# Kernel optimization log

Hardware: AMD Instinct MI355X
Metric: run time of the kernel (lower is better)

Reference implementation:

```python
import jax, jax.numpy as jnp
import numpy as np

VOCAB, B, T, H, E = 32000, 32, 128, 128, 128

def setup_inputs() -> dict:
    key = jax.random.key(0)
    ks = jax.random.split(key, 10)
    s = 0.05
    return {
        "inputs": jax.random.randint(ks[0], (B, T), 0, VOCAB, dtype=jnp.int32),
        "emb": jax.random.normal(ks[1], (VOCAB, E), jnp.float32) * s,
        "W0": jax.random.normal(ks[2], (E, 4 * H), jnp.float32) * s,
        "U0": jax.random.normal(ks[3], (H, 4 * H), jnp.float32) * s,
        "b0": jnp.zeros((4 * H,), jnp.float32),
        "W1": jax.random.normal(ks[4], (H, 4 * H), jnp.float32) * s,
        "U1": jax.random.normal(ks[5], (H, 4 * H), jnp.float32) * s,
        "b1": jnp.zeros((4 * H,), jnp.float32),
        "Wd": jax.random.normal(ks[6], (H, VOCAB), jnp.float32) * s,
        "bd": jnp.zeros((VOCAB,), jnp.float32),
    }

def _lstm_cell(x, h, c, W, U, b):
    # Keras LSTMCell gate order: i, f, c(candidate), o
    z = x @ W + h @ U + b  # [B, 4H]
    zi, zf, zc, zo = jnp.split(z, 4, axis=-1)
    i = jax.nn.sigmoid(zi)
    f = jax.nn.sigmoid(zf)
    o = jax.nn.sigmoid(zo)
    c_new = f * c + i * jnp.tanh(zc)
    h_new = o * jnp.tanh(c_new)
    return h_new, c_new

def reference(inputs, emb, W0, U0, b0, W1, U1, b1, Wd, bd):
    x = emb[inputs]  # [B, T, E]
    xt = jnp.transpose(x, (1, 0, 2))  # [T, B, E]
    zeros = jnp.zeros((x.shape[0], H), x.dtype)
    init = (zeros, zeros, zeros, zeros)  # h0, c0, h1, c1

    def step(carry, x_t):
        h0, c0, h1, c1 = carry
        h0, c0 = _lstm_cell(x_t, h0, c0, W0, U0, b0)
        h1, c1 = _lstm_cell(h0, h1, c1, W1, U1, b1)
        return (h0, c0, h1, c1), h1

    _, ys = jax.lax.scan(step, init, xt)  # ys: [T, B, H]
    y = jnp.transpose(ys, (1, 0, 2))  # [B, T, H]
    logits = y @ Wd + bd  # [B, T, VOCAB]
    return logits
```

## Files before the change

kernel.cpp:

```cpp
#include <hip/hip_runtime.h>
#include <math.h>

#define BB 32
#define TT 128
#define EE 128
#define HD 128
#define G4 512
#define NV 32000

typedef _Float16 f16x2  __attribute__((ext_vector_type(2)));
typedef _Float16 f16x4v __attribute__((ext_vector_type(4)));
typedef _Float16 f16x8  __attribute__((ext_vector_type(8)));
typedef float    f32x4  __attribute__((ext_vector_type(4)));

__global__ __launch_bounds__(256) void k_prep(
    const int* __restrict__ inputs, const float* __restrict__ emb,
    const float* __restrict__ W0, const float* __restrict__ b0,
    float* __restrict__ Z0x,
    const float* __restrict__ Wd, _Float16* __restrict__ Whi, _Float16* __restrict__ Wlo)
{
    if (blockIdx.x < 2000) {
        if (Whi == nullptr) return;
        const int g = blockIdx.x * 256 + threadIdx.x;
        const int chunk = g >> 6;
        const int lane = g & 63;
        const int ntile = chunk >> 2;
        const int kstep = chunk & 3;
        const int n = ntile * 16 + (lane & 15);
        const int kb = kstep * 32 + (lane >> 4) * 8;
        _Float16 hi[8], lo[8];
        #pragma unroll
        for (int j = 0; j < 8; ++j) {
            float v = Wd[(size_t)(kb + j) * NV + n];
            hi[j] = (_Float16)v;
            lo[j] = (_Float16)(v - (float)hi[j]);
        }
        *(float4*)&Whi[(size_t)chunk * 512 + lane * 8] = *(const float4*)hi;
        *(float4*)&Wlo[(size_t)chunk * 512 + lane * 8] = *(const float4*)lo;
        return;
    }
    __shared__ float xs[8][EE];
    const int r0 = (blockIdx.x - 2000) * 8;
    const int tid = threadIdx.x;
    for (int i = tid; i < 8 * EE; i += 256) {
        int r = i >> 7, e = i & 127;
        int tok = inputs[r0 + r];
        xs[r][e] = emb[tok * EE + e];
    }
    __syncthreads();
    const int c2 = tid * 2;
    float2 bb2 = *(const float2*)&b0[c2];
    float acc[8][2];
    #pragma unroll
    for (int r = 0; r < 8; ++r) { acc[r][0] = bb2.x; acc[r][1] = bb2.y; }
    for (int e = 0; e < EE; ++e) {
        float2 w = *(const float2*)&W0[e * G4 + c2];
        #pragma unroll
        for (int r = 0; r < 8; ++r) {
            float x = xs[r][e];
            acc[r][0] = fmaf(x, w.x, acc[r][0]);
            acc[r][1] = fmaf(x, w.y, acc[r][1]);
        }
    }
    #pragma unroll
    for (int r = 0; r < 8; ++r) {
        float2 o2; o2.x = acc[r][0]; o2.y = acc[r][1];
        *(float2*)&Z0x[(size_t)(r0 + r) * G4 + c2] = o2;
    }
}

__device__ __forceinline__ float sigf(float x) {
    return __builtin_amdgcn_rcpf(1.f + __builtin_amdgcn_exp2f(x * -1.44269504088896f));
}
__device__ __forceinline__ float tanh_f(float x) {
    return 1.f - 2.f * __builtin_amdgcn_rcpf(1.f + __builtin_amdgcn_exp2f(x * 2.88539008177793f));
}
__device__ __forceinline__ f16x8 ldfrag(const float* __restrict__ M, int col, int k0) {
    f16x8 v;
    #pragma unroll
    for (int j = 0; j < 8; ++j) v[j] = (_Float16)M[(size_t)(k0 + j) * G4 + col];
    return v;
}

#define REP8(X) X(0) X(1) X(2) X(3) X(4) X(5) X(6) X(7)

#define MFMA(acc, a, b) acc = __builtin_amdgcn_mfma_f32_16x16x32_f16(a, b, acc, 0, 0, 0)

#define DECLF(n) f16x8 u0_##n##_0, u0_##n##_1, u0_##n##_2, u0_##n##_3, \
                       w1_##n##_0, w1_##n##_1, w1_##n##_2, w1_##n##_3, \
                       u1_##n##_0, u1_##n##_1, u1_##n##_2, u1_##n##_3;

#define LOADF(n) { const int cn = wc0 + (n) * 16 + lo16; \
    u0_##n##_0 = ldfrag(U0, cn, khi);      u0_##n##_1 = ldfrag(U0, cn, 32 + khi); \
    u0_##n##_2 = ldfrag(U0, cn, 64 + khi); u0_##n##_3 = ldfrag(U0, cn, 96 + khi); \
    w1_##n##_0 = ldfrag(W1, cn, khi);      w1_##n##_1 = ldfrag(W1, cn, 32 + khi); \
    w1_##n##_2 = ldfrag(W1, cn, 64 + khi); w1_##n##_3 = ldfrag(W1, cn, 96 + khi); \
    asm("" : "+a"(w1_##n##_0), "+a"(w1_##n##_1), "+a"(w1_##n##_2), "+a"(w1_##n##_3)); \
    u1_##n##_0 = ldfrag(U1, cn, khi);      u1_##n##_1 = ldfrag(U1, cn, 32 + khi); \
    u1_##n##_2 = ldfrag(U1, cn, 64 + khi); u1_##n##_3 = ldfrag(U1, cn, 96 + khi); \
    asm("" : "+a"(u1_##n##_0), "+a"(u1_##n##_1), "+a"(u1_##n##_2), "+a"(u1_##n##_3)); }

#define PA(n) { f32x4 acc = {0.f, 0.f, 0.f, 0.f}; \
    MFMA(acc, ha0, u0_##n##_0); MFMA(acc, ha1, u0_##n##_1); \
    MFMA(acc, ha2, u0_##n##_2); MFMA(acc, ha3, u0_##n##_3); \
    if (lane < 32) { const int cw = wc0 + (n) * 16 + lo16; const int br = (lane >> 4) * 4; \
        zbuf[br + 0][cw] = acc[0]; zbuf[br + 1][cw] = acc[1]; \
        zbuf[br + 2][cw] = acc[2]; zbuf[br + 3][cw] = acc[3]; } }

#define PC(n) { f32x4 acc = {0.f, 0.f, 0.f, 0.f}; \
    MFMA(acc, ha0, w1_##n##_0); MFMA(acc, ha1, w1_##n##_1); \
    MFMA(acc, ha2, w1_##n##_2); MFMA(acc, ha3, w1_##n##_3); \
    MFMA(acc, hb0, u1_##n##_0); MFMA(acc, hb1, u1_##n##_1); \
    MFMA(acc, hb2, u1_##n##_2); MFMA(acc, hb3, u1_##n##_3); \
    if (lane < 32) { const int cw = wc0 + (n) * 16 + lo16; const int br = (lane >> 4) * 4; \
        zbuf[br + 0][cw] = acc[0]; zbuf[br + 1][cw] = acc[1]; \
        zbuf[br + 2][cw] = acc[2]; zbuf[br + 3][cw] = acc[3]; } }

#define GT0(K, ZI, ZF, ZC, ZO) { \
    float ig = sigf(ZI), fg = sigf(ZF), og = sigf(ZO), gg = tanh_f(ZC); \
    float cn = fg * c0v[K] + ig * gg; c0v[K] = cn; hv[K] = (_Float16)(og * tanh_f(cn)); }

#define GT1(K, ZI, ZF, ZC, ZO, YO) { \
    float ig = sigf(ZI), fg = sigf(ZF), og = sigf(ZO), gg = tanh_f(ZC); \
    float cn = fg * c1v[K] + ig * gg; c1v[K] = cn; float hn = og * tanh_f(cn); \
    hv[K] = (_Float16)hn; YO = hn; }

__global__ __launch_bounds__(256, 1) void k_lstm_m(
    const float* __restrict__ Z0x,
    const float* __restrict__ U0, const float* __restrict__ W1,
    const float* __restrict__ U1, const float* __restrict__ b1,
    float* __restrict__ y)
{
    const int tid  = threadIdx.x;
    const int lane = tid & 63;
    const int wc0  = (tid >> 6) * 128;
    const int lo16 = lane & 15;
    const int khi  = (lane >> 4) * 8;
    const int B0   = blockIdx.x * 8;

    __shared__ float     zbuf[8][516];
    __shared__ _Float16  h0p[16][136];
    __shared__ _Float16  h1p[16][136];

    REP8(DECLF)
    REP8(LOADF)

    const int bq  = tid >> 5;
    const int h0i = (tid & 31) * 4;
    const float* zx_base = Z0x + ((size_t)(B0 + bq) * TT) * G4;
    float*       y_base  = y   + ((size_t)(B0 + bq) * TT) * HD + h0i;

    const float4 b1_i = *(const float4*)&b1[0 * 128 + h0i];
    const float4 b1_f = *(const float4*)&b1[1 * 128 + h0i];
    const float4 b1_c = *(const float4*)&b1[2 * 128 + h0i];
    const float4 b1_o = *(const float4*)&b1[3 * 128 + h0i];

    for (int i = tid; i < 16 * 136; i += 256) {
        ((_Float16*)h0p)[i] = (_Float16)0.f;
        ((_Float16*)h1p)[i] = (_Float16)0.f;
    }
    f32x4 c0v = {0.f, 0.f, 0.f, 0.f};
    f32x4 c1v = {0.f, 0.f, 0.f, 0.f};
    __syncthreads();

    for (int t = 0; t < TT; ++t) {
        const float* zx = zx_base + (size_t)t * G4;
        const float4 x_i = *(const float4*)&zx[0 * 128 + h0i];
        const float4 x_f = *(const float4*)&zx[1 * 128 + h0i];
        const float4 x_c = *(const float4*)&zx[2 * 128 + h0i];
        const float4 x_o = *(const float4*)&zx[3 * 128 + h0i];

        {
            f16x8 ha0 = *(const f16x8*)&h0p[lo16][khi];
            f16x8 ha1 = *(const f16x8*)&h0p[lo16][32 + khi];
            f16x8 ha2 = *(const f16x8*)&h0p[lo16][64 + khi];
            f16x8 ha3 = *(const f16x8*)&h0p[lo16][96 + khi];
            REP8(PA)
        }
        __syncthreads();

        {
            const float4 zi4 = *(const float4*)&zbuf[bq][0 * 128 + h0i];
            const float4 zf4 = *(const float4*)&zbuf[bq][1 * 128 + h0i];
            const float4 zc4 = *(const float4*)&zbuf[bq][2 * 128 + h0i];
            const float4 zo4 = *(const float4*)&zbuf[bq][3 * 128 + h0i];
            f16x4v hv;
            GT0(0, zi4.x + x_i.x, zf4.x + x_f.x, zc4.x + x_c.x, zo4.x + x_o.x)
            GT0(1, zi4.y + x_i.y, zf4.y + x_f.y, zc4.y + x_c.y, zo4.y + x_o.y)
            GT0(2, zi4.z + x_i.z, zf4.z + x_f.z, zc4.z + x_c.z, zo4.z + x_o.z)
            GT0(3, zi4.w + x_i.w, zf4.w + x_f.w, zc4.w + x_c.w, zo4.w + x_o.w)
            *(f16x4v*)&h0p[bq][h0i] = hv;
        }
        __syncthreads();

        {
            f16x8 ha0 = *(const f16x8*)&h0p[lo16][khi];
            f16x8 ha1 = *(const f16x8*)&h0p[lo16][32 + khi];
            f16x8 ha2 = *(const f16x8*)&h0p[lo16][64 + khi];
            f16x8 ha3 = *(const f16x8*)&h0p[lo16][96 + khi];
            f16x8 hb0 = *(const f16x8*)&h1p[lo16][khi];
            f16x8 hb1 = *(const f16x8*)&h1p[lo16][32 + khi];
            f16x8 hb2 = *(const f16x8*)&h1p[lo16][64 + khi];
            f16x8 hb3 = *(const f16x8*)&h1p[lo16][96 + khi];
            REP8(PC)
        }
        __syncthreads();

        {
            const float4 zi4 = *(const float4*)&zbuf[bq][0 * 128 + h0i];
            const float4 zf4 = *(const float4*)&zbuf[bq][1 * 128 + h0i];
            const float4 zc4 = *(const float4*)&zbuf[bq][2 * 128 + h0i];
            const float4 zo4 = *(const float4*)&zbuf[bq][3 * 128 + h0i];
            f16x4v hv; float4 yv;
            GT1(0, zi4.x + b1_i.x, zf4.x + b1_f.x, zc4.x + b1_c.x, zo4.x + b1_o.x, yv.x)
            GT1(1, zi4.y + b1_i.y, zf4.y + b1_f.y, zc4.y + b1_c.y, zo4.y + b1_o.y, yv.y)
            GT1(2, zi4.z + b1_i.z, zf4.z + b1_f.z, zc4.z + b1_c.z, zo4.z + b1_o.z, yv.z)
            GT1(3, zi4.w + b1_i.w, zf4.w + b1_f.w, zc4.w + b1_c.w, zo4.w + b1_o.w, yv.w)
            *(f16x4v*)&h1p[bq][h0i] = hv;
            *(float4*)(y_base + (size_t)t * HD) = yv;
        }
        __syncthreads();
    }
}

__global__ __launch_bounds__(256) void k_ysplit(
    const float* __restrict__ y, _Float16* __restrict__ yhi, _Float16* __restrict__ ylo)
{
    const int g = blockIdx.x * 256 + threadIdx.x;
    const int chunk = g >> 6;
    const int lane = g & 63;
    const int mtile = chunk >> 2;
    const int kstep = chunk & 3;
    const int row = mtile * 16 + (lane & 15);
    const int kb = kstep * 32 + (lane >> 4) * 8;
    _Float16 hi[8], lo[8];
    #pragma unroll
    for (int j = 0; j < 8; ++j) {
        float v = y[(size_t)row * HD + kb + j];
        hi[j] = (_Float16)v;
        lo[j] = (_Float16)(v - (float)hi[j]);
    }
    *(float4*)&yhi[(size_t)chunk * 512 + lane * 8] = *(const float4*)hi;
    *(float4*)&ylo[(size_t)chunk * 512 + lane * 8] = *(const float4*)lo;
}

__global__ __launch_bounds__(256) void k_dense_mfma(
    const _Float16* __restrict__ yhi, const _Float16* __restrict__ ylo,
    const _Float16* __restrict__ Whi, const _Float16* __restrict__ Wlo,
    const float* __restrict__ bd, float* __restrict__ out)
{
    const int tid = threadIdx.x;
    const int w = tid >> 6;
    const int lane = tid & 63;
    const int mtile = blockIdx.x * 4 + w;
    const int nt0 = blockIdx.y * 20;

    f16x8 Ah[4], Al[4];
    #pragma unroll
    for (int k = 0; k < 4; ++k) {
        Ah[k] = *(const f16x8*)&yhi[(size_t)(mtile * 4 + k) * 512 + lane * 8];
        Al[k] = *(const f16x8*)&ylo[(size_t)(mtile * 4 + k) * 512 + lane * 8];
    }

    const int m0 = mtile * 16;
    const int r0 = (lane >> 4) * 4;

    for (int nt = 0; nt < 20; ++nt) {
        const int ntile = nt0 + nt;
        const size_t cbb = (size_t)ntile * 4 * 512 + lane * 8;
        f16x8 Bh[4], Bl[4];
        #pragma unroll
        for (int k = 0; k < 4; ++k) {
            Bh[k] = *(const f16x8*)&Whi[cbb + k * 512];
            Bl[k] = *(const f16x8*)&Wlo[cbb + k * 512];
        }
        f32x4 acc0 = {0.f, 0.f, 0.f, 0.f};
        f32x4 acc1 = {0.f, 0.f, 0.f, 0.f};
        #pragma unroll
        for (int k = 0; k < 4; ++k) {
            acc0 = __builtin_amdgcn_mfma_f32_16x16x32_f16(Ah[k], Bh[k], acc0, 0, 0, 0);
            acc1 = __builtin_amdgcn_mfma_f32_16x16x32_f16(Ah[k], Bl[k], acc1, 0, 0, 0);
            acc1 = __builtin_amdgcn_mfma_f32_16x16x32_f16(Al[k], Bh[k], acc1, 0, 0, 0);
        }
        const int col = ntile * 16 + (lane & 15);
        const float bias = bd[col];
        #pragma unroll
        for (int reg = 0; reg < 4; ++reg) {
            out[(size_t)(m0 + r0 + reg) * NV + col] = acc0[reg] + acc1[reg] + bias;
        }
    }
}

__global__ __launch_bounds__(256) void k_dense(
    const float* __restrict__ y, const float* __restrict__ Wd,
    const float* __restrict__ bd, float* __restrict__ out)
{
    __shared__ float ys[64 * HD];
    const int r0 = blockIdx.x * 64;
    const int v0 = blockIdx.y * 128;
    const int tid = threadIdx.x;
    for (int idx = tid; idx < 64 * HD; idx += 256) ys[idx] = y[(size_t)r0 * HD + idx];
    __syncthreads();
    const int tx = tid & 31;
    const int ty = tid >> 5;
    const int v = v0 + tx * 4;
    float4 bd4 = *(const float4*)&bd[v];
    float acc[8][4] = {};
    const float* yrow = &ys[(ty * 8) * HD];
    #pragma unroll 4
    for (int e = 0; e < HD; ++e) {
        float4 wv = *(const float4*)&Wd[(size_t)e * NV + v];
        #pragma unroll
        for (int j = 0; j < 8; ++j) {
            float yv = yrow[j * HD + e];
            acc[j][0] = fmaf(yv, wv.x, acc[j][0]);
            acc[j][1] = fmaf(yv, wv.y, acc[j][1]);
            acc[j][2] = fmaf(yv, wv.z, acc[j][2]);
            acc[j][3] = fmaf(yv, wv.w, acc[j][3]);
        }
    }
    #pragma unroll
    for (int j = 0; j < 8; ++j) {
        int rr = r0 + ty * 8 + j;
        float4 o4;
        o4.x = acc[j][0] + bd4.x;
        o4.y = acc[j][1] + bd4.y;
        o4.z = acc[j][2] + bd4.z;
        o4.w = acc[j][3] + bd4.w;
        *(float4*)&out[(size_t)rr * NV + v] = o4;
    }
}

extern "C" void kernel_launch(void* const* d_in, const int* in_sizes, int n_in,
                              void* d_out, int out_size, void* d_ws, size_t ws_size,
                              hipStream_t stream)
{
    const int*   inputs = (const int*)  d_in[0];
    const float* emb    = (const float*)d_in[1];
    const float* W0     = (const float*)d_in[2];
    const float* U0     = (const float*)d_in[3];
    const float* b0     = (const float*)d_in[4];
    const float* W1     = (const float*)d_in[5];
    const float* U1     = (const float*)d_in[6];
    const float* b1     = (const float*)d_in[7];
    const float* Wd     = (const float*)d_in[8];
    const float* bd     = (const float*)d_in[9];
    float* out = (float*)d_out;

    const size_t Z0X_B = (size_t)8 * 1024 * 1024;
    const size_t YY_B  = (size_t)2 * 1024 * 1024;
    const size_t WSP_B = (size_t)8000 * 512 * 2;
    const size_t YSP_B = (size_t)1024 * 512 * 2;
    const size_t NEED  = Z0X_B + YY_B + 2 * WSP_B + 2 * YSP_B + 4096;

    char* ws = (char*)d_ws;

    if (ws_size >= NEED) {
        float*     Z0x = (float*)ws;
        float*     yy  = (float*)(ws + Z0X_B);
        _Float16*  Whi = (_Float16*)(ws + Z0X_B + YY_B);
        _Float16*  Wlo = (_Float16*)(ws + Z0X_B + YY_B + WSP_B);
        _Float16*  yhi = (_Float16*)(ws + Z0X_B + YY_B + 2 * WSP_B);
        _Float16*  ylo = (_Float16*)(ws + Z0X_B + YY_B + 2 * WSP_B + YSP_B);

        k_prep<<<2512, 256, 0, stream>>>(inputs, emb, W0, b0, Z0x, Wd, Whi, Wlo);
        k_lstm_m<<<4, 256, 0, stream>>>(Z0x, U0, W1, U1, b1, yy);
        k_ysplit<<<256, 256, 0, stream>>>(yy, yhi, ylo);
        k_dense_mfma<<<dim3(64, 100), 256, 0, stream>>>(yhi, ylo, Whi, Wlo, bd, out);
    } else {
        float* yy = (float*)ws;
        size_t out_bytes = (size_t)out_size * sizeof(float);
        float* Z0x = (float*)((char*)d_out + out_bytes - Z0X_B);

        k_prep<<<2512, 256, 0, stream>>>(inputs, emb, W0, b0, Z0x,
                                         Wd, nullptr, nullptr);
        k_lstm_m<<<4, 256, 0, stream>>>(Z0x, U0, W1, U1, b1, yy);
        k_dense<<<dim3(64, 250), 256, 0, stream>>>(yy, Wd, bd, out);
    }
}
```

Baseline: 606.8 us.

## Compute LSTM gates in registers with column-aligned ownership and double-buffered h

```diff
diff --git a/kernel.cpp b/kernel.cpp
--- a/kernel.cpp
+++ b/kernel.cpp
@@ -83,14 +83,16 @@
 }
 
 #define REP8(X) X(0) X(1) X(2) X(3) X(4) X(5) X(6) X(7)
-
 #define MFMA(acc, a, b) acc = __builtin_amdgcn_mfma_f32_16x16x32_f16(a, b, acc, 0, 0, 0)
+#define TSTR (TT * G4)
 
 #define DECLF(n) f16x8 u0_##n##_0, u0_##n##_1, u0_##n##_2, u0_##n##_3, \
                        w1_##n##_0, w1_##n##_1, w1_##n##_2, w1_##n##_3, \
-                       u1_##n##_0, u1_##n##_1, u1_##n##_2, u1_##n##_3;
-
-#define LOADF(n) { const int cn = wc0 + (n) * 16 + lo16; \
+                       u1_##n##_0, u1_##n##_1, u1_##n##_2, u1_##n##_3; \
+                 f32x4 aU1_##n, aZ_##n; float b1c_##n; int col_##n;
+
+#define LOADF(n) { col_##n = ((n) >> 1) * 128 + wu + ((n) & 1) * 16 + lo16; \
+    const int cn = col_##n; \
     u0_##n##_0 = ldfrag(U0, cn, khi);      u0_##n##_1 = ldfrag(U0, cn, 32 + khi); \
     u0_##n##_2 = ldfrag(U0, cn, 64 + khi); u0_##n##_3 = ldfrag(U0, cn, 96 + khi); \
     w1_##n##_0 = ldfrag(W1, cn, khi);      w1_##n##_1 = ldfrag(W1, cn, 32 + khi); \
@@ -98,34 +100,37 @@
     asm("" : "+a"(w1_##n##_0), "+a"(w1_##n##_1), "+a"(w1_##n##_2), "+a"(w1_##n##_3)); \
     u1_##n##_0 = ldfrag(U1, cn, khi);      u1_##n##_1 = ldfrag(U1, cn, 32 + khi); \
     u1_##n##_2 = ldfrag(U1, cn, 64 + khi); u1_##n##_3 = ldfrag(U1, cn, 96 + khi); \
-    asm("" : "+a"(u1_##n##_0), "+a"(u1_##n##_1), "+a"(u1_##n##_2), "+a"(u1_##n##_3)); }
-
-#define PA(n) { f32x4 acc = {0.f, 0.f, 0.f, 0.f}; \
-    MFMA(acc, ha0, u0_##n##_0); MFMA(acc, ha1, u0_##n##_1); \
-    MFMA(acc, ha2, u0_##n##_2); MFMA(acc, ha3, u0_##n##_3); \
-    if (lane < 32) { const int cw = wc0 + (n) * 16 + lo16; const int br = (lane >> 4) * 4; \
-        zbuf[br + 0][cw] = acc[0]; zbuf[br + 1][cw] = acc[1]; \
-        zbuf[br + 2][cw] = acc[2]; zbuf[br + 3][cw] = acc[3]; } }
-
-#define PC(n) { f32x4 acc = {0.f, 0.f, 0.f, 0.f}; \
-    MFMA(acc, ha0, w1_##n##_0); MFMA(acc, ha1, w1_##n##_1); \
-    MFMA(acc, ha2, w1_##n##_2); MFMA(acc, ha3, w1_##n##_3); \
-    MFMA(acc, hb0, u1_##n##_0); MFMA(acc, hb1, u1_##n##_1); \
-    MFMA(acc, hb2, u1_##n##_2); MFMA(acc, hb3, u1_##n##_3); \
-    if (lane < 32) { const int cw = wc0 + (n) * 16 + lo16; const int br = (lane >> 4) * 4; \
-        zbuf[br + 0][cw] = acc[0]; zbuf[br + 1][cw] = acc[1]; \
-        zbuf[br + 2][cw] = acc[2]; zbuf[br + 3][cw] = acc[3]; } }
-
-#define GT0(K, ZI, ZF, ZC, ZO) { \
-    float ig = sigf(ZI), fg = sigf(ZF), og = sigf(ZO), gg = tanh_f(ZC); \
-    float cn = fg * c0v[K] + ig * gg; c0v[K] = cn; hv[K] = (_Float16)(og * tanh_f(cn)); }
-
-#define GT1(K, ZI, ZF, ZC, ZO, YO) { \
-    float ig = sigf(ZI), fg = sigf(ZF), og = sigf(ZO), gg = tanh_f(ZC); \
-    float cn = fg * c1v[K] + ig * gg; c1v[K] = cn; float hn = og * tanh_f(cn); \
-    hv[K] = (_Float16)hn; YO = hn; }
-
-__global__ __launch_bounds__(256, 1) void k_lstm_m(
+    asm("" : "+a"(u1_##n##_0), "+a"(u1_##n##_1), "+a"(u1_##n##_2), "+a"(u1_##n##_3)); \
+    b1c_##n = b1[cn]; }
+
+#define PU1(n) { f32x4 a = {0.f, 0.f, 0.f, 0.f}; \
+    MFMA(a, hb0, u1_##n##_0); MFMA(a, hb1, u1_##n##_1); \
+    MFMA(a, hb2, u1_##n##_2); MFMA(a, hb3, u1_##n##_3); aU1_##n = a; }
+
+#define PU0(n) { const float* zc = zxt + col_##n; f32x4 a; \
+    a[0] = zc[0]; a[1] = zc[TSTR]; a[2] = zc[2 * TSTR]; a[3] = zc[3 * TSTR]; \
+    MFMA(a, ha0, u0_##n##_0); MFMA(a, ha1, u0_##n##_1); \
+    MFMA(a, ha2, u0_##n##_2); MFMA(a, ha3, u0_##n##_3); aZ_##n = a; }
+
+#define PW1(n) { f32x4 a = {b1c_##n, b1c_##n, b1c_##n, b1c_##n}; \
+    MFMA(a, ha0, w1_##n##_0); MFMA(a, ha1, w1_##n##_1); \
+    MFMA(a, ha2, w1_##n##_2); MFMA(a, ha3, w1_##n##_3); \
+    aZ_##n = a + aU1_##n; }
+
+#define G0R(nI, nF, nC, nO, CS, h, r) { \
+    float ig = sigf(aZ_##nI[r]), fg = sigf(aZ_##nF[r]), og = sigf(aZ_##nO[r]); \
+    float gg = tanh_f(aZ_##nC[r]); \
+    float cn = fg * CS[r] + ig * gg; CS[r] = cn; \
+    h0c[bq4 + r][wu + lo16 + 16 * (h)] = (_Float16)(og * tanh_f(cn)); }
+
+#define G1R(nI, nF, nC, nO, CS, h, r) { \
+    float ig = sigf(aZ_##nI[r]), fg = sigf(aZ_##nF[r]), og = sigf(aZ_##nO[r]); \
+    float gg = tanh_f(aZ_##nC[r]); \
+    float cn = fg * CS[r] + ig * gg; CS[r] = cn; float hn = og * tanh_f(cn); \
+    h1c[bq4 + r][wu + lo16 + 16 * (h)] = (_Float16)hn; \
+    yb[(size_t)(r) * TT * HD + (size_t)t * HD + 16 * (h)] = hn; }
+
+__global__ __launch_bounds__(256, 1) void k_lstm_m2(
     const float* __restrict__ Z0x,
     const float* __restrict__ U0, const float* __restrict__ W1,
     const float* __restrict__ U1, const float* __restrict__ b1,
@@ -133,91 +138,71 @@
 {
     const int tid  = threadIdx.x;
     const int lane = tid & 63;
-    const int wc0  = (tid >> 6) * 128;
+    const int wu   = (tid >> 6) * 32;
     const int lo16 = lane & 15;
     const int khi  = (lane >> 4) * 8;
     const int B0   = blockIdx.x * 8;
-
-    __shared__ float     zbuf[8][516];
-    __shared__ _Float16  h0p[16][136];
-    __shared__ _Float16  h1p[16][136];
+    const int bq4  = (lane >> 4) * 4;
+    const int xr   = ((lane >> 4) & 1) * 4;
+
+    __shared__ _Float16 h0p[2][16][136];
+    __shared__ _Float16 h1p[2][16][136];
 
     REP8(DECLF)
     REP8(LOADF)
 
-    const int bq  = tid >> 5;
-    const int h0i = (tid & 31) * 4;
-    const float* zx_base = Z0x + ((size_t)(B0 + bq) * TT) * G4;
-    float*       y_base  = y   + ((size_t)(B0 + bq) * TT) * HD + h0i;
-
-    const float4 b1_i = *(const float4*)&b1[0 * 128 + h0i];
-    const float4 b1_f = *(const float4*)&b1[1 * 128 + h0i];
-    const float4 b1_c = *(const float4*)&b1[2 * 128 + h0i];
-    const float4 b1_o = *(const float4*)&b1[3 * 128 + h0i];
-
-    for (int i = tid; i < 16 * 136; i += 256) {
-        ((_Float16*)h0p)[i] = (_Float16)0.f;
-        ((_Float16*)h1p)[i] = (_Float16)0.f;
-    }
-    f32x4 c0v = {0.f, 0.f, 0.f, 0.f};
-    f32x4 c1v = {0.f, 0.f, 0.f, 0.f};
+    const float* zx0 = Z0x + ((size_t)(B0 + xr) * TT) * G4;
+    float* yb = y + ((size_t)(B0 + bq4) * TT) * HD + wu + lo16;
+
+    f32x4 c0a = {0.f,0.f,0.f,0.f}, c0b = {0.f,0.f,0.f,0.f};
+    f32x4 c1a = {0.f,0.f,0.f,0.f}, c1b = {0.f,0.f,0.f,0.f};
+
+    for (int i = tid; i < 2 * 16 * 136; i += 256) {
+        (&h0p[0][0][0])[i] = (_Float16)0.f;
+        (&h1p[0][0][0])[i] = (_Float16)0.f;
+    }
     __syncthreads();
 
     for (int t = 0; t < TT; ++t) {
-        const float* zx = zx_base + (size_t)t * G4;
-        const float4 x_i = *(const float4*)&zx[0 * 128 + h0i];
-        const float4 x_f = *(const float4*)&zx[1 * 128 + h0i];
-        const float4 x_c = *(const float4*)&zx[2 * 128 + h0i];
-        const float4 x_o = *(const float4*)&zx[3 * 128 + h0i];
+        const int p = t & 1;
+        const _Float16 (*h0r)[136] = h0p[p ^ 1];
+        const _Float16 (*h1r)[136] = h1p[p ^ 1];
+        _Float16 (*h0c)[136] = h0p[p];
+        _Float16 (*h1c)[136] = h1p[p];
+        const float* zxt = zx0 + (size_t)t * G4;
 
         {
-            f16x8 ha0 = *(const f16x8*)&h0p[lo16][khi];
-            f16x8 ha1 = *(const f16x8*)&h0p[lo16][32 + khi];
-            f16x8 ha2 = *(const f16x8*)&h0p[lo16][64 + khi];
-            f16x8 ha3 = *(const f16x8*)&h0p[lo16][96 + khi];
-            REP8(PA)
+            f16x8 hb0 = *(const f16x8*)&h1r[lo16][khi];
+            f16x8 hb1 = *(const f16x8*)&h1r[lo16][32 + khi];
+            f16x8 hb2 = *(const f16x8*)&h1r[lo16][64 + khi];
+            f16x8 hb3 = *(const f16x8*)&h1r[lo16][96 + khi];
+            REP8(PU1)
+            f16x8 ha0 = *(const f16x8*)&h0r[lo16][khi];
+            f16x8 ha1 = *(const f16x8*)&h0r[lo16][32 + khi];
+            f16x8 ha2 = *(const f16x8*)&h0r[lo16][64 + khi];
+            f16x8 ha3 = *(const f16x8*)&h0r[lo16][96 + khi];
+            REP8(PU0)
+        }
+        if (lane < 32) {
+            G0R(0, 2, 4, 6, c0a, 0, 0) G0R(0, 2, 4, 6, c0a, 0, 1)
+            G0R(0, 2, 4, 6, c0a, 0, 2) G0R(0, 2, 4, 6, c0a, 0, 3)
+            G0R(1, 3, 5, 7, c0b, 1, 0) G0R(1, 3, 5, 7, c0b, 1, 1)
+            G0R(1, 3, 5, 7, c0b, 1, 2) G0R(1, 3, 5, 7, c0b, 1, 3)
         }
         __syncthreads();
 
         {
-            const float4 zi4 = *(const float4*)&zbuf[bq][0 * 128 + h0i];
-            const float4 zf4 = *(const float4*)&zbuf[bq][1 * 128 + h0i];
-            const float4 zc4 = *(const float4*)&zbuf[bq][2 * 128 + h0i];
-            const float4 zo4 = *(const float4*)&zbuf[bq][3 * 128 + h0i];
-            f16x4v hv;
-            GT0(0, zi4.x + x_i.x, zf4.x + x_f.x, zc4.x + x_c.x, zo4.x + x_o.x)
-            GT0(1, zi4.y + x_i.y, zf4.y + x_f.y, zc4.y + x_c.y, zo4.y + x_o.y)
-            GT0(2, zi4.z + x_i.z, zf4.z + x_f.z, zc4.z + x_c.z, zo4.z + x_o.z)
-            GT0(3, zi4.w + x_i.w, zf4.w + x_f.w, zc4.w + x_c.w, zo4.w + x_o.w)
-            *(f16x4v*)&h0p[bq][h0i] = hv;
-        }
-        __syncthreads();
-
-        {
-            f16x8 ha0 = *(const f16x8*)&h0p[lo16][khi];
-            f16x8 ha1 = *(const f16x8*)&h0p[lo16][32 + khi];
-            f16x8 ha2 = *(const f16x8*)&h0p[lo16][64 + khi];
-            f16x8 ha3 = *(const f16x8*)&h0p[lo16][96 + khi];
-            f16x8 hb0 = *(const f16x8*)&h1p[lo16][khi];
-            f16x8 hb1 = *(const f16x8*)&h1p[lo16][32 + khi];
-            f16x8 hb2 = *(const f16x8*)&h1p[lo16][64 + khi];
-            f16x8 hb3 = *(const f16x8*)&h1p[lo16][96 + khi];
-            REP8(PC)
-        }
-        __syncthreads();
-
-        {
-            const float4 zi4 = *(const float4*)&zbuf[bq][0 * 128 + h0i];
-            const float4 zf4 = *(const float4*)&zbuf[bq][1 * 128 + h0i];
-            const float4 zc4 = *(const float4*)&zbuf[bq][2 * 128 + h0i];
-            const float4 zo4 = *(const float4*)&zbuf[bq][3 * 128 + h0i];
-            f16x4v hv; float4 yv;
-            GT1(0, zi4.x + b1_i.x, zf4.x + b1_f.x, zc4.x + b1_c.x, zo4.x + b1_o.x, yv.x)
-            GT1(1, zi4.y + b1_i.y, zf4.y + b1_f.y, zc4.y + b1_c.y, zo4.y + b1_o.y, yv.y)
-            GT1(2, zi4.z + b1_i.z, zf4.z + b1_f.z, zc4.z + b1_c.z, zo4.z + b1_o.z, yv.z)
-            GT1(3, zi4.w + b1_i.w, zf4.w + b1_f.w, zc4.w + b1_c.w, zo4.w + b1_o.w, yv.w)
-            *(f16x4v*)&h1p[bq][h0i] = hv;
-            *(float4*)(y_base + (size_t)t * HD) = yv;
+            f16x8 ha0 = *(const f16x8*)&h0c[lo16][khi];
+            f16x8 ha1 = *(const f16x8*)&h0c[lo16][32 + khi];
+            f16x8 ha2 = *(const f16x8*)&h0c[lo16][64 + khi];
+            f16x8 ha3 = *(const f16x8*)&h0c[lo16][96 + khi];
+            REP8(PW1)
+        }
+        if (lane < 32) {
+            G1R(0, 2, 4, 6, c1a, 0, 0) G1R(0, 2, 4, 6, c1a, 0, 1)
+            G1R(0, 2, 4, 6, c1a, 0, 2) G1R(0, 2, 4, 6, c1a, 0, 3)
+            G1R(1, 3, 5, 7, c1b, 1, 0) G1R(1, 3, 5, 7, c1b, 1, 1)
+            G1R(1, 3, 5, 7, c1b, 1, 2) G1R(1, 3, 5, 7, c1b, 1, 3)
         }
         __syncthreads();
     }
@@ -364,7 +349,7 @@
         _Float16*  ylo = (_Float16*)(ws + Z0X_B + YY_B + 2 * WSP_B + YSP_B);
 
         k_prep<<<2512, 256, 0, stream>>>(inputs, emb, W0, b0, Z0x, Wd, Whi, Wlo);
-        k_lstm_m<<<4, 256, 0, stream>>>(Z0x, U0, W1, U1, b1, yy);
+        k_lstm_m2<<<4, 256, 0, stream>>>(Z0x, U0, W1, U1, b1, yy);
         k_ysplit<<<256, 256, 0, stream>>>(yy, yhi, ylo);
         k_dense_mfma<<<dim3(64, 100), 256, 0, stream>>>(yhi, ylo, Whi, Wlo, bd, out);
     } else {
@@ -374,7 +359,7 @@
 
         k_prep<<<2512, 256, 0, stream>>>(inputs, emb, W0, b0, Z0x,
                                          Wd, nullptr, nullptr);
-        k_lstm_m<<<4, 256, 0, stream>>>(Z0x, U0, W1, U1, b1, yy);
+        k_lstm_m2<<<4, 256, 0, stream>>>(Z0x, U0, W1, U1, b1, yy);
         k_dense<<<dim3(64, 250), 256, 0, stream>>>(yy, Wd, bd, out);
     }
 }
```

Measured after the change: 946.2 us. 1.56x slower.

## Overlap Wd split with LSTM recurrence and retile dense MFMA to reuse B

Applied to the files above, without the earlier changes.

```diff
diff --git a/kernel.cpp b/kernel.cpp
--- a/kernel.cpp
+++ b/kernel.cpp
@@ -13,34 +13,13 @@
 typedef _Float16 f16x8  __attribute__((ext_vector_type(8)));
 typedef float    f32x4  __attribute__((ext_vector_type(4)));
 
-__global__ __launch_bounds__(256) void k_prep(
+__global__ __launch_bounds__(256) void k_embed(
     const int* __restrict__ inputs, const float* __restrict__ emb,
     const float* __restrict__ W0, const float* __restrict__ b0,
-    float* __restrict__ Z0x,
-    const float* __restrict__ Wd, _Float16* __restrict__ Whi, _Float16* __restrict__ Wlo)
-{
-    if (blockIdx.x < 2000) {
-        if (Whi == nullptr) return;
-        const int g = blockIdx.x * 256 + threadIdx.x;
-        const int chunk = g >> 6;
-        const int lane = g & 63;
-        const int ntile = chunk >> 2;
-        const int kstep = chunk & 3;
-        const int n = ntile * 16 + (lane & 15);
-        const int kb = kstep * 32 + (lane >> 4) * 8;
-        _Float16 hi[8], lo[8];
-        #pragma unroll
-        for (int j = 0; j < 8; ++j) {
-            float v = Wd[(size_t)(kb + j) * NV + n];
-            hi[j] = (_Float16)v;
-            lo[j] = (_Float16)(v - (float)hi[j]);
-        }
-        *(float4*)&Whi[(size_t)chunk * 512 + lane * 8] = *(const float4*)hi;
-        *(float4*)&Wlo[(size_t)chunk * 512 + lane * 8] = *(const float4*)lo;
-        return;
-    }
+    float* __restrict__ Z0x)
+{
     __shared__ float xs[8][EE];
-    const int r0 = (blockIdx.x - 2000) * 8;
+    const int r0 = blockIdx.x * 8;
     const int tid = threadIdx.x;
     for (int i = tid; i < 8 * EE; i += 256) {
         int r = i >> 7, e = i & 127;
@@ -83,7 +62,6 @@
 }
 
 #define REP8(X) X(0) X(1) X(2) X(3) X(4) X(5) X(6) X(7)
-
 #define MFMA(acc, a, b) acc = __builtin_amdgcn_mfma_f32_16x16x32_f16(a, b, acc, 0, 0, 0)
 
 #define DECLF(n) f16x8 u0_##n##_0, u0_##n##_1, u0_##n##_2, u0_##n##_3, \
@@ -125,13 +103,36 @@
     float cn = fg * c1v[K] + ig * gg; c1v[K] = cn; float hn = og * tanh_f(cn); \
     hv[K] = (_Float16)hn; YO = hn; }
 
-__global__ __launch_bounds__(256, 1) void k_lstm_m(
+__global__ __launch_bounds__(256, 1) void k_lstm_mw(
     const float* __restrict__ Z0x,
     const float* __restrict__ U0, const float* __restrict__ W1,
     const float* __restrict__ U1, const float* __restrict__ b1,
-    float* __restrict__ y)
+    float* __restrict__ y,
+    const float* __restrict__ Wd, _Float16* __restrict__ Whi, _Float16* __restrict__ Wlo)
 {
     const int tid  = threadIdx.x;
+
+    if (blockIdx.x >= 4) {
+        if (Whi == nullptr) return;
+        const int g = (blockIdx.x - 4) * 256 + tid;
+        const int chunk = g >> 6;
+        const int ln = g & 63;
+        const int ntile = chunk >> 2;
+        const int kstep = chunk & 3;
+        const int n = ntile * 16 + (ln & 15);
+        const int kb = kstep * 32 + (ln >> 4) * 8;
+        _Float16 hi[8], lo[8];
+        #pragma unroll
+        for (int j = 0; j < 8; ++j) {
+            float v = Wd[(size_t)(kb + j) * NV + n];
+            hi[j] = (_Float16)v;
+            lo[j] = (_Float16)(v - (float)hi[j]);
+        }
+        *(float4*)&Whi[(size_t)chunk * 512 + ln * 8] = *(const float4*)hi;
+        *(float4*)&Wlo[(size_t)chunk * 512 + ln * 8] = *(const float4*)lo;
+        return;
+    }
+
     const int lane = tid & 63;
     const int wc0  = (tid >> 6) * 128;
     const int lo16 = lane & 15;
@@ -244,49 +245,78 @@
     *(float4*)&ylo[(size_t)chunk * 512 + lane * 8] = *(const float4*)lo;
 }
 
-__global__ __launch_bounds__(256) void k_dense_mfma(
+__global__ __launch_bounds__(256) void k_dense_mfma2(
     const _Float16* __restrict__ yhi, const _Float16* __restrict__ ylo,
     const _Float16* __restrict__ Whi, const _Float16* __restrict__ Wlo,
     const float* __restrict__ bd, float* __restrict__ out)
 {
-    const int tid = threadIdx.x;
-    const int w = tid >> 6;
+    const int tid  = threadIdx.x;
+    const int w    = tid >> 6;
     const int lane = tid & 63;
-    const int mtile = blockIdx.x * 4 + w;
-    const int nt0 = blockIdx.y * 20;
-
-    f16x8 Ah[4], Al[4];
-    #pragma unroll
-    for (int k = 0; k < 4; ++k) {
-        Ah[k] = *(const f16x8*)&yhi[(size_t)(mtile * 4 + k) * 512 + lane * 8];
-        Al[k] = *(const f16x8*)&ylo[(size_t)(mtile * 4 + k) * 512 + lane * 8];
-    }
-
-    const int m0 = mtile * 16;
-    const int r0 = (lane >> 4) * 4;
-
-    for (int nt = 0; nt < 20; ++nt) {
-        const int ntile = nt0 + nt;
-        const size_t cbb = (size_t)ntile * 4 * 512 + lane * 8;
-        f16x8 Bh[4], Bl[4];
+    const int nt0  = blockIdx.y * 16 + w * 4;
+    const int mt0  = blockIdx.x * 32;
+
+    f16x8 Bh[4][4], Bl[4][4];
+    #pragma unroll
+    for (int n = 0; n < 4; ++n) {
+        const size_t cb = (size_t)(nt0 + n) * 4 * 512 + lane * 8;
         #pragma unroll
         for (int k = 0; k < 4; ++k) {
-            Bh[k] = *(const f16x8*)&Whi[cbb + k * 512];
-            Bl[k] = *(const f16x8*)&Wlo[cbb + k * 512];
-        }
-        f32x4 acc0 = {0.f, 0.f, 0.f, 0.f};
-        f32x4 acc1 = {0.f, 0.f, 0.f, 0.f};
+            Bh[n][k] = *(const f16x8*)&Whi[cb + k * 512];
+            Bl[n][k] = *(const f16x8*)&Wlo[cb + k * 512];
+        }
+    }
+    float bias[4];
+    #pragma unroll
+    for (int n = 0; n < 4; ++n) bias[n] = bd[(nt0 + n) * 16 + (lane & 15)];
+
+    const int r0 = (lane >> 4) * 4;
+
+    for (int mt = 0; mt < 32; ++mt) {
+        const int mtile = mt0 + mt;
+        const size_t ab = (size_t)mtile * 4 * 512 + lane * 8;
+
+        f32x4 acc0[4] = {{0,0,0,0},{0,0,0,0},{0,0,0,0},{0,0,0,0}};
+        f32x4 acc1[4] = {{0,0,0,0},{0,0,0,0},{0,0,0,0},{0,0,0,0}};
+
+        {
+            f16x8 A0 = *(const f16x8*)&yhi[ab];
+            f16x8 A1 = *(const f16x8*)&yhi[ab + 512];
+            f16x8 A2 = *(const f16x8*)&yhi[ab + 1024];
+            f16x8 A3 = *(const f16x8*)&yhi[ab + 1536];
+            #pragma unroll
+            for (int n = 0; n < 4; ++n) {
+                acc0[n] = __builtin_amdgcn_mfma_f32_16x16x32_f16(A0, Bh[n][0], acc0[n], 0, 0, 0);
+                acc0[n] = __builtin_amdgcn_mfma_f32_16x16x32_f16(A1, Bh[n][1], acc0[n], 0, 0, 0);
+                acc0[n] = __builtin_amdgcn_mfma_f32_16x16x32_f16(A2, Bh[n][2], acc0[n], 0, 0, 0);
+                acc0[n] = __builtin_amdgcn_mfma_f32_16x16x32_f16(A3, Bh[n][3], acc0[n], 0, 0, 0);
+                acc1[n] = __builtin_amdgcn_mfma_f32_16x16x32_f16(A0, Bl[n][0], acc1[n], 0, 0, 0);
+                acc1[n] = __builtin_amdgcn_mfma_f32_16x16x32_f16(A1, Bl[n][1], acc1[n], 0, 0, 0);
+                acc1[n] = __builtin_amdgcn_mfma_f32_16x16x32_f16(A2, Bl[n][2], acc1[n], 0, 0, 0);
+                acc1[n] = __builtin_amdgcn_mfma_f32_16x16x32_f16(A3, Bl[n][3], acc1[n], 0, 0, 0);
+            }
+        }
+        {
+            f16x8 A0 = *(const f16x8*)&ylo[ab];
+            f16x8 A1 = *(const f16x8*)&ylo[ab + 512];
+            f16x8 A2 = *(const f16x8*)&ylo[ab + 1024];
+            f16x8 A3 = *(const f16x8*)&ylo[ab + 1536];
+            #pragma unroll
+            for (int n = 0; n < 4; ++n) {
+                acc1[n] = __builtin_amdgcn_mfma_f32_16x16x32_f16(A0, Bh[n][0], acc1[n], 0, 0, 0);
+                acc1[n] = __builtin_amdgcn_mfma_f32_16x16x32_f16(A1, Bh[n][1], acc1[n], 0, 0, 0);
+                acc1[n] = __builtin_amdgcn_mfma_f32_16x16x32_f16(A2, Bh[n][2], acc1[n], 0, 0, 0);
+                acc1[n] = __builtin_amdgcn_mfma_f32_16x16x32_f16(A3, Bh[n][3], acc1[n], 0, 0, 0);
+            }
+        }
+        const int m0 = mtile * 16;
         #pragma unroll
-        for (int k = 0; k < 4; ++k) {
-            acc0 = __builtin_amdgcn_mfma_f32_16x16x32_f16(Ah[k], Bh[k], acc0, 0, 0, 0);
-            acc1 = __builtin_amdgcn_mfma_f32_16x16x32_f16(Ah[k], Bl[k], acc1, 0, 0, 0);
-            acc1 = __builtin_amdgcn_mfma_f32_16x16x32_f16(Al[k], Bh[k], acc1, 0, 0, 0);
-        }
-        const int col = ntile * 16 + (lane & 15);
-        const float bias = bd[col];
-        #pragma unroll
-        for (int reg = 0; reg < 4; ++reg) {
-            out[(size_t)(m0 + r0 + reg) * NV + col] = acc0[reg] + acc1[reg] + bias;
+        for (int n = 0; n < 4; ++n) {
+            const int col = (nt0 + n) * 16 + (lane & 15);
+            #pragma unroll
+            for (int reg = 0; reg < 4; ++reg) {
+                out[(size_t)(m0 + r0 + reg) * NV + col] = acc0[n][reg] + acc1[n][reg] + bias[n];
+            }
         }
     }
 }
@@ -363,18 +393,18 @@
         _Float16*  yhi = (_Float16*)(ws + Z0X_B + YY_B + 2 * WSP_B);
         _Float16*  ylo = (_Float16*)(ws + Z0X_B + YY_B + 2 * WSP_B + YSP_B);
 
-        k_prep<<<2512, 256, 0, stream>>>(inputs, emb, W0, b0, Z0x, Wd, Whi, Wlo);
-        k_lstm_m<<<4, 256, 0, stream>>>(Z0x, U0, W1, U1, b1, yy);
+        k_embed<<<512, 256, 0, stream>>>(inputs, emb, W0, b0, Z0x);
+        k_lstm_mw<<<2004, 256, 0, stream>>>(Z0x, U0, W1, U1, b1, yy, Wd, Whi, Wlo);
         k_ysplit<<<256, 256, 0, stream>>>(yy, yhi, ylo);
-        k_dense_mfma<<<dim3(64, 100), 256, 0, stream>>>(yhi, ylo, Whi, Wlo, bd, out);
+        k_dense_mfma2<<<dim3(8, 125), 256, 0, stream>>>(yhi, ylo, Whi, Wlo, bd, out);
     } else {
         float* yy = (float*)ws;
         size_t out_bytes = (size_t)out_size * sizeof(float);
         float* Z0x = (float*)((char*)d_out + out_bytes - Z0X_B);
 
-        k_prep<<<2512, 256, 0, stream>>>(inputs, emb, W0, b0, Z0x,
-                                         Wd, nullptr, nullptr);
-        k_lstm_m<<<4, 256, 0, stream>>>(Z0x, U0, W1, U1, b1, yy);
+        k_embed<<<512, 256, 0, stream>>>(inputs, emb, W0, b0, Z0x);
+        k_lstm_mw<<<2004, 256, 0, stream>>>(Z0x, U0, W1, U1, b1, yy,
+                                            Wd, nullptr, nullptr);
         k_dense<<<dim3(64, 250), 256, 0, stream>>>(yy, Wd, bd, out);
     }
 }
```

Measured after the change: 549.6 us. -9.4%, faster.
